# Performance work log

Hardware: AMD Instinct MI355X
Metric: run time of the kernel (lower is better)

The kernel has to match this reference:

```python
import jax, jax.numpy as jnp
import numpy as np

D = 768
H = 16
DH = D // H  # 48
SCALE = 1.0 / np.sqrt(DH).astype(np.float32)
EPS = 1e-3  # keras LayerNormalization default epsilon
NEG = -1e9


def setup_inputs() -> dict:
    key = jax.random.key(0)
    ks = jax.random.split(key, 10)
    B, S = 4, 2048
    q = jax.random.normal(ks[0], (B, S, D), dtype=jnp.float32)
    k = jax.random.normal(ks[1], (B, S, D), dtype=jnp.float32)
    v = jax.random.normal(ks[2], (B, S, D), dtype=jnp.float32)
    # Dense projection params (glorot-ish scale)
    w_std = 1.0 / np.sqrt(D)
    Wq = jax.random.normal(ks[3], (D, D), dtype=jnp.float32) * w_std
    Wk = jax.random.normal(ks[4], (D, D), dtype=jnp.float32) * w_std
    Wv = jax.random.normal(ks[5], (D, D), dtype=jnp.float32) * w_std
    bq = jnp.zeros((D,), jnp.float32)
    bk = jnp.zeros((D,), jnp.float32)
    bv = jnp.zeros((D,), jnp.float32)
    gamma = jnp.ones((D,), jnp.float32)
    beta = jnp.zeros((D,), jnp.float32)
    return {"q": q, "k": k, "v": v, "Wq": Wq, "bq": bq, "Wk": Wk, "bk": bk,
            "Wv": Wv, "bv": bv, "gamma": gamma, "beta": beta}


def reference(q, k, v, Wq, bq, Wk, bk, Wv, bv, gamma, beta):
    use_causal = True  # exercise the causal-mask path
    B, S, _ = q.shape
    # Projections, then split into heads (tf.split on last axis == reshape)
    Q = (q @ Wq + bq).reshape(B, S, H, DH)
    K = (k @ Wk + bk).reshape(B, S, H, DH)
    V = (v @ Wv + bv).reshape(B, S, H, DH)
    # scores: [B, H, Sq, Sk]
    scores = jnp.einsum('bqhd,bkhd->bhqk', Q, K) * SCALE
    if use_causal:
        qi = jnp.arange(S)[:, None]
        ki = jnp.arange(S)[None, :]
        mask = jnp.where(qi >= ki, 0.0, NEG).astype(scores.dtype)
        scores = scores + mask
    attn = jax.nn.softmax(scores, axis=-1)
    out = jnp.einsum('bhqk,bkhd->bqhd', attn, V).reshape(B, S, D)
    # LayerNorm over last dim
    mu = jnp.mean(out, axis=-1, keepdims=True)
    var = jnp.mean(jnp.square(out - mu), axis=-1, keepdims=True)
    return (out - mu) * jax.lax.rsqrt(var + EPS) * gamma + beta
```

## Files before the change

### kernel.cpp

```cpp
#include <hip/hip_runtime.h>
#include <hip/hip_bf16.h>


#define DMODEL 768
#define NHEAD  16
#define DHEAD  48
#define SEQ    2048
#define NBATCH 4
#define NROWS  (NBATCH * SEQ)
#define QSCALE (0.14433756729740643f * 1.4426950408889634f)

typedef __bf16 bf16x8 __attribute__((ext_vector_type(8)));
typedef float  f32x4  __attribute__((ext_vector_type(4)));
typedef float  f32x16 __attribute__((ext_vector_type(16)));
typedef unsigned int u32x4 __attribute__((ext_vector_type(4)));

#if __has_builtin(__builtin_amdgcn_exp2f)
#define EXP2(x) __builtin_amdgcn_exp2f(x)
#else
#define EXP2(x) exp2f(x)
#endif

static __device__ __forceinline__ unsigned int pk2(float lo, float hi) {
    unsigned short a = __builtin_bit_cast(unsigned short, (__bf16)lo);
    unsigned short b = __builtin_bit_cast(unsigned short, (__bf16)hi);
    return ((unsigned int)b << 16) | a;
}

static __device__ __forceinline__ __hip_bfloat16 bfc(float x) {
    return __float2bfloat16(x);
}

__global__ __launch_bounds__(256) void prep(
    const float* __restrict__ Wq,
    const float* __restrict__ Wk,
    const float* __restrict__ Wv,
    const float* __restrict__ xq,
    const float* __restrict__ xk,
    const float* __restrict__ xv,
    __hip_bfloat16* __restrict__ Wt,
    __hip_bfloat16* __restrict__ Xbq,
    __hip_bfloat16* __restrict__ Xbk,
    __hip_bfloat16* __restrict__ Xbv)
{
    int bid = blockIdx.x;
    if (bid < 1728) {
        __shared__ __hip_bfloat16 tile[32][33];
        int mat = bid / 576;
        int t   = bid - mat * 576;
        int tr  = t / 24, tc = t - (t / 24) * 24;
        const float* W = (mat == 0) ? Wq : (mat == 1) ? Wk : Wv;
        __hip_bfloat16* O = Wt + (size_t)mat * DMODEL * DMODEL;
        int tx = threadIdx.x & 31, ty = threadIdx.x >> 5;
#pragma unroll
        for (int i = 0; i < 32; i += 8)
            tile[ty + i][tx] = __float2bfloat16(W[(size_t)(tr * 32 + ty + i) * DMODEL + tc * 32 + tx]);
        __syncthreads();
#pragma unroll
        for (int i = 0; i < 32; i += 8)
            O[(size_t)(tc * 32 + ty + i) * DMODEL + tr * 32 + tx] = tile[tx][ty + i];
    } else {
        int b2  = bid - 1728;
        int mat = b2 / 3072;
        int r   = b2 - mat * 3072;
        const float* X = (mat == 0) ? xq : (mat == 1) ? xk : xv;
        __hip_bfloat16* O = (mat == 0) ? Xbq : (mat == 1) ? Xbk : Xbv;
        size_t off = (size_t)r * 2048 + threadIdx.x * 8;
        float4 f0 = *(const float4*)(X + off);
        float4 f1 = *(const float4*)(X + off + 4);
        unsigned int w0 = pk2(f0.x, f0.y), w1 = pk2(f0.z, f0.w);
        unsigned int w2 = pk2(f1.x, f1.y), w3 = pk2(f1.z, f1.w);
        u32x4 pv; pv[0] = w0; pv[1] = w1; pv[2] = w2; pv[3] = w3;
        *(u32x4*)(O + off) = pv;
    }
}

__global__ __launch_bounds__(512, 4) void qkv_proj(
    const __hip_bfloat16* __restrict__ Xbq,
    const __hip_bfloat16* __restrict__ Xbk,
    const __hip_bfloat16* __restrict__ Xbv,
    const __hip_bfloat16* __restrict__ Wt,
    const float* __restrict__ bq,
    const float* __restrict__ bk,
    const float* __restrict__ bv,
    __hip_bfloat16* __restrict__ Qr,
    __hip_bfloat16* __restrict__ Kr,
    __hip_bfloat16* __restrict__ Vt)
{
    __shared__ __hip_bfloat16 Abuf[3][8192];
    __shared__ __hip_bfloat16 Bbuf[2][4096];

    int tid  = threadIdx.x;
    int w    = tid >> 6, lane = tid & 63;
    int l16  = lane & 15, quad = lane >> 4;
    int wm   = w >> 1, wn = w & 1;

    int xcd = blockIdx.x & 7, s = blockIdx.x >> 3;
    int nt  = s % 6;
    int idx = (s / 6) * 8 + xcd;
    int mat = idx >> 5, mt = idx & 31;
    int m0  = mt * 256, n0 = nt * 128;

    const __hip_bfloat16* X = (mat == 0) ? Xbq : (mat == 1) ? Xbk : Xbv;
    const __hip_bfloat16* W = Wt + (size_t)mat * DMODEL * DMODEL;
    const float* bias       = (mat == 0) ? bq : (mat == 1) ? bk : bv;

    int sr = tid >> 2;
    int sc = ((tid & 3) ^ ((tid >> 3) & 3)) * 8;
    const __hip_bfloat16* ga0 = X + (size_t)(m0 + sr) * DMODEL + sc;
    const __hip_bfloat16* ga1 = X + (size_t)(m0 + 128 + sr) * DMODEL + sc;
    const __hip_bfloat16* gb  = W + (size_t)(n0 + sr) * DMODEL + sc;

#define GLD(gp_, lp_) __builtin_amdgcn_global_load_lds(                        \
        (const __attribute__((address_space(1))) void*)(gp_),                  \
        (__attribute__((address_space(3))) void*)(lp_), 16, 0, 0)

    int swz  = (quad ^ ((l16 >> 1) & 3)) * 8;
    int aoff = (wm * 64 + l16) * 32 + swz;
    int boff = (wn * 64 + l16) * 32 + swz;

    f32x4 acc[4][4] = {};

    GLD(gb,       &Bbuf[0][tid * 8]);
    GLD(ga0,      &Abuf[0][tid * 8]);
    GLD(ga1,      &Abuf[0][4096 + tid * 8]);
    GLD(ga0 + 32, &Abuf[1][tid * 8]);
    GLD(ga1 + 32, &Abuf[1][4096 + tid * 8]);
    asm volatile("s_waitcnt vmcnt(2)" ::: "memory");
    asm volatile("s_barrier" ::: "memory");

    int abuf = 0, bbuf = 0, abS = 2;
    const __hip_bfloat16* gbS  = gb  + 32;
    const __hip_bfloat16* ga0S = ga0 + 64;
    const __hip_bfloat16* ga1S = ga1 + 64;

    for (int kt = 0; kt < 24; ++kt) {
        const __hip_bfloat16* LA = Abuf[abuf];
        const __hip_bfloat16* LB = Bbuf[bbuf];

        bf16x8 a[4], bA[2];
#pragma unroll
        for (int m_ = 0; m_ < 4; ++m_)
            a[m_] = *(const bf16x8*)&LA[aoff + m_ * 512];
        bA[0] = *(const bf16x8*)&LB[boff];
        bA[1] = *(const bf16x8*)&LB[boff + 512];

        if (kt < 23) { GLD(gbS, &Bbuf[bbuf ^ 1][tid * 8]); gbS += 32; }
        if (kt < 22) {
            GLD(ga0S, &Abuf[abS][tid * 8]);
            GLD(ga1S, &Abuf[abS][4096 + tid * 8]);
            ga0S += 32; ga1S += 32;
        }

        asm volatile("s_barrier" ::: "memory");
        __builtin_amdgcn_s_setprio(1);
#pragma unroll
        for (int m_ = 0; m_ < 4; ++m_) {
            acc[m_][0] = __builtin_amdgcn_mfma_f32_16x16x32_bf16(a[m_], bA[0], acc[m_][0], 0, 0, 0);
            acc[m_][1] = __builtin_amdgcn_mfma_f32_16x16x32_bf16(a[m_], bA[1], acc[m_][1], 0, 0, 0);
        }
        __builtin_amdgcn_s_setprio(0);
        asm volatile("s_barrier" ::: "memory");

        bf16x8 bB[2];
        bB[0] = *(const bf16x8*)&LB[boff + 1024];
        bB[1] = *(const bf16x8*)&LB[boff + 1536];

        if (kt < 22) asm volatile("s_waitcnt vmcnt(2)" ::: "memory");
        else         asm volatile("s_waitcnt vmcnt(0)" ::: "memory");
        asm volatile("s_barrier" ::: "memory");
        __builtin_amdgcn_s_setprio(1);
#pragma unroll
        for (int m_ = 0; m_ < 4; ++m_) {
            acc[m_][2] = __builtin_amdgcn_mfma_f32_16x16x32_bf16(a[m_], bB[0], acc[m_][2], 0, 0, 0);
            acc[m_][3] = __builtin_amdgcn_mfma_f32_16x16x32_bf16(a[m_], bB[1], acc[m_][3], 0, 0, 0);
        }
        __builtin_amdgcn_s_setprio(0);
        asm volatile("s_barrier" ::: "memory");

        abuf = (abuf == 2) ? 0 : abuf + 1;
        abS  = (abS  == 2) ? 0 : abS  + 1;
        bbuf ^= 1;
    }
#undef GLD

    int colb = n0 + wn * 64 + l16;
    float bc0 = bias[colb];
    float bc1 = bias[colb + 16];
    float bc2 = bias[colb + 32];
    float bc3 = bias[colb + 48];
    if (mat == 0) {
#pragma unroll
        for (int i = 0; i < 4; ++i) {
            int row0 = m0 + wm * 64 + i * 16 + quad * 4;
#pragma unroll
            for (int r = 0; r < 4; ++r) {
                __hip_bfloat16* p = Qr + (size_t)(row0 + r) * DMODEL + colb;
                p[0]  = bfc((acc[i][0][r] + bc0) * QSCALE);
                p[16] = bfc((acc[i][1][r] + bc1) * QSCALE);
                p[32] = bfc((acc[i][2][r] + bc2) * QSCALE);
                p[48] = bfc((acc[i][3][r] + bc3) * QSCALE);
            }
        }
    } else if (mat == 1) {
#pragma unroll
        for (int i = 0; i < 4; ++i) {
            int row0 = m0 + wm * 64 + i * 16 + quad * 4;
#pragma unroll
            for (int r = 0; r < 4; ++r) {
                __hip_bfloat16* p = Kr + (size_t)(row0 + r) * DMODEL + colb;
                p[0]  = bfc(acc[i][0][r] + bc0);
                p[16] = bfc(acc[i][1][r] + bc1);
                p[32] = bfc(acc[i][2][r] + bc2);
                p[48] = bfc(acc[i][3][r] + bc3);
            }
        }
    } else {
#pragma unroll
        for (int j = 0; j < 4; ++j) {
            int col = colb + j * 16;
            float bc = (j == 0) ? bc0 : (j == 1) ? bc1 : (j == 2) ? bc2 : bc3;
            int h = col / 48, dh = col - h * 48;
#pragma unroll
            for (int i = 0; i < 4; ++i) {
                int row0 = m0 + wm * 64 + i * 16 + quad * 4;
                int bb = row0 >> 11, s0 = row0 & 2047;
                unsigned int lo = pk2(acc[i][j][0] + bc, acc[i][j][1] + bc);
                unsigned int hi = pk2(acc[i][j][2] + bc, acc[i][j][3] + bc);
                uint2 pw; pw.x = lo; pw.y = hi;
                *(uint2*)(Vt + ((size_t)(bb * NHEAD + h) * DHEAD + dh) * SEQ + s0) = pw;
            }
        }
    }
}

__global__ __launch_bounds__(256, 3) void attn(
    const __hip_bfloat16* __restrict__ Qr,
    const __hip_bfloat16* __restrict__ Kr,
    const __hip_bfloat16* __restrict__ Vt,
    __hip_bfloat16* __restrict__ Ao)
{
    __shared__ __hip_bfloat16 Ks[2][64][64];
    __shared__ __hip_bfloat16 Vs[2][64][64];

    int tid  = threadIdx.x;
    int w    = tid >> 6, lane = tid & 63;
    int l31  = lane & 31;
    int half = lane >> 5;
    bool hb  = half != 0;
    int bh   = blockIdx.x & 63;
    int qt   = 15 - (blockIdx.x >> 6);
    int q0   = qt * 128;
    int b    = bh >> 4, h = bh & 15;
    size_t rowbase = (size_t)b * SEQ;

    const __hip_bfloat16* Qp = Qr + rowbase * DMODEL + h * DHEAD;
    const __hip_bfloat16* Kp = Kr + rowbase * DMODEL + h * DHEAD;
    const __hip_bfloat16* Vp = Vt + (size_t)bh * DHEAD * SEQ;

    {
        int zbuf = tid >> 7, zi = tid & 127;
        int zr = 48 + (zi >> 3), zsl = zi & 7;
        unsigned int v = (zr == 48) ? 0x3F803F80u : 0u;
        u32x4 pv; pv[0] = v; pv[1] = v; pv[2] = v; pv[3] = v;
        *(u32x4*)&Vs[zbuf][zr][(zsl ^ (zr & 7)) * 8] = pv;
    }

    int q0w = q0 + w * 32;
    bf16x8 bQ0, bQ1, bQ2;
    {
        const __hip_bfloat16* qp = Qp + (size_t)(q0w + l31) * DMODEL + half * 8;
        bQ0 = *(const bf16x8*)(qp);
        bQ1 = *(const bf16x8*)(qp + 16);
        bQ2 = *(const bf16x8*)(qp + 32);
    }

    int kr1 = tid / 6,          ksl1 = tid - kr1 * 6;
    int kr2 = (tid + 256) / 6,  ksl2 = (tid + 256) - kr2 * 6;
    int vd1 = tid >> 3,         vsl1 = tid & 7;
    int vd2 = (tid + 256) >> 3, vsl2 = tid & 7;
    int kso1 = (ksl1 ^ (kr1 & 7)) * 8;
    int kso2 = (ksl2 ^ (kr2 & 7)) * 8;
    int vso1 = (vsl1 ^ (vd1 & 7)) * 8;
    int vso2 = (vsl2 ^ (vd2 & 7)) * 8;

    const __hip_bfloat16* pK1 = Kp + (size_t)kr1 * DMODEL + ksl1 * 8;
    const __hip_bfloat16* pK2 = Kp + (size_t)kr2 * DMODEL + ksl2 * 8;
    const __hip_bfloat16* pV1 = Vp + (size_t)vd1 * SEQ + vsl1 * 8;
    const __hip_bfloat16* pV2 = Vp + (size_t)vd2 * SEQ + vsl2 * 8;

    uint4 kv1, kv2, vv1, vv2;

#define ATTN_LOAD() {                                                           \
        kv1 = *(const uint4*)pK1;                                               \
        vv1 = *(const uint4*)pV1;                                               \
        if (tid < 128) {                                                        \
            kv2 = *(const uint4*)pK2;                                           \
            vv2 = *(const uint4*)pV2;                                           \
        }                                                                       \
        pK1 += 64 * DMODEL; pK2 += 64 * DMODEL; pV1 += 64; pV2 += 64; }

#define ATTN_STORE(buf_) {                                                      \
        *(uint4*)&Ks[buf_][kr1][kso1] = kv1;                                    \
        *(uint4*)&Vs[buf_][vd1][vso1] = vv1;                                    \
        if (tid < 128) {                                                        \
            *(uint4*)&Ks[buf_][kr2][kso2] = kv2;                                \
            *(uint4*)&Vs[buf_][vd2][vso2] = vv2;                                \
        } }

#define MFMA32(A_, B_, C_) __builtin_amdgcn_mfma_f32_32x32x16_bf16(A_, B_, C_, 0, 0, 0)

    f32x16 O1 = {}, O2 = {};
    const f32x16 z16 = {};

    int ktmax = 2 * qt + 1;
    ATTN_LOAD();
    ATTN_STORE(0);
    ATTN_LOAD();
    __syncthreads();

    for (int kt = 0; kt <= ktmax; ++kt) {
        int buf = kt & 1;
        int k0  = kt * 64;
        if (kt + 1 <= ktmax) ATTN_STORE(buf ^ 1);
        if (kt + 2 <= ktmax) ATTN_LOAD();

#pragma unroll
        for (int kc = 0; kc < 2; ++kc) {
            int kbase = k0 + kc * 32;
            if (kbase <= q0w + 31) {
                int krow = kc * 32 + l31;
                int ksw  = krow & 7;
                bf16x8 aK0 = *(const bf16x8*)&Ks[buf][krow][((0 + half) ^ ksw) * 8];
                bf16x8 aK1 = *(const bf16x8*)&Ks[buf][krow][((2 + half) ^ ksw) * 8];
                bf16x8 aK2 = *(const bf16x8*)&Ks[buf][krow][((4 + half) ^ ksw) * 8];

                __builtin_amdgcn_s_setprio(1);
                f32x16 s_;
                s_ = MFMA32(aK0, bQ0, z16);
                s_ = MFMA32(aK1, bQ1, s_);
                s_ = MFMA32(aK2, bQ2, s_);
                __builtin_amdgcn_s_setprio(0);

                if (kbase + 31 > q0w) {
                    int qg = q0w + l31;
                    int kb = kbase + (hb ? 4 : 0);
#pragma unroll
                    for (int r = 0; r < 16; ++r) {
                        int kl = (r & 3) + 8 * (r >> 2);
                        if (kb + kl > qg) s_[r] = -1e30f;
                    }
                }

                unsigned int p0, p1, p2, p3, p4, p5, p6, p7;
                {
                    float e0 = EXP2(s_[0]),  e1 = EXP2(s_[1]);
                    float e2 = EXP2(s_[2]),  e3 = EXP2(s_[3]);
                    float e4 = EXP2(s_[4]),  e5 = EXP2(s_[5]);
                    float e6 = EXP2(s_[6]),  e7 = EXP2(s_[7]);
                    float e8 = EXP2(s_[8]),  e9 = EXP2(s_[9]);
                    float ea = EXP2(s_[10]), eb = EXP2(s_[11]);
                    float ec = EXP2(s_[12]), ed = EXP2(s_[13]);
                    float ee = EXP2(s_[14]), ef = EXP2(s_[15]);
                    p0 = pk2(e0, e1); p1 = pk2(e2, e3);
                    p2 = pk2(e4, e5); p3 = pk2(e6, e7);
                    p4 = pk2(e8, e9); p5 = pk2(ea, eb);
                    p6 = pk2(ec, ed); p7 = pk2(ee, ef);
                }

                u32x4 F0w, F1w;
#if __has_builtin(__builtin_amdgcn_permlane32_swap)
                {
                    typedef unsigned int u32x2 __attribute__((ext_vector_type(2)));
                    u32x2 r0 = __builtin_amdgcn_permlane32_swap(p0, p2, false, false);
                    u32x2 r1 = __builtin_amdgcn_permlane32_swap(p1, p3, false, false);
                    u32x2 r2 = __builtin_amdgcn_permlane32_swap(p4, p6, false, false);
                    u32x2 r3 = __builtin_amdgcn_permlane32_swap(p5, p7, false, false);
                    F0w[0] = r0[0]; F0w[1] = r1[0]; F0w[2] = r0[1]; F0w[3] = r1[1];
                    F1w[0] = r2[0]; F1w[1] = r3[0]; F1w[2] = r2[1]; F1w[3] = r3[1];
                }
#else
                {
                    unsigned int sx0 = __shfl_xor(hb ? p0 : p2, 32, 64);
                    unsigned int sx1 = __shfl_xor(hb ? p1 : p3, 32, 64);
                    unsigned int sx2 = __shfl_xor(hb ? p4 : p6, 32, 64);
                    unsigned int sx3 = __shfl_xor(hb ? p5 : p7, 32, 64);
                    F0w[0] = hb ? sx0 : p0;  F0w[1] = hb ? sx1 : p1;
                    F0w[2] = hb ? p2  : sx0; F0w[3] = hb ? p3  : sx1;
                    F1w[0] = hb ? sx2 : p4;  F1w[1] = hb ? sx3 : p5;
                    F1w[2] = hb ? p6  : sx2; F1w[3] = hb ? p7  : sx3;
                }
#endif
                bf16x8 F0 = __builtin_bit_cast(bf16x8, F0w);
                bf16x8 F1 = __builtin_bit_cast(bf16x8, F1w);

                int vr0 = l31, vr1 = 32 + l31;
                int vw0 = vr0 & 7, vw1 = vr1 & 7;
                bf16x8 bV00 = *(const bf16x8*)&Vs[buf][vr0][((kc * 4 + 0 + half) ^ vw0) * 8];
                bf16x8 bV01 = *(const bf16x8*)&Vs[buf][vr1][((kc * 4 + 0 + half) ^ vw1) * 8];
                bf16x8 bV10 = *(const bf16x8*)&Vs[buf][vr0][((kc * 4 + 2 + half) ^ vw0) * 8];
                bf16x8 bV11 = *(const bf16x8*)&Vs[buf][vr1][((kc * 4 + 2 + half) ^ vw1) * 8];

                __builtin_amdgcn_s_setprio(1);
                O1 = MFMA32(F0, bV00, O1);
                O2 = MFMA32(F0, bV01, O2);
                O1 = MFMA32(F1, bV10, O1);
                O2 = MFMA32(F1, bV11, O2);
                __builtin_amdgcn_s_setprio(0);
            }
        }

        asm volatile("s_waitcnt lgkmcnt(0)" ::: "memory");
        __builtin_amdgcn_s_barrier();
        asm volatile("" ::: "memory");
    }

    int lsrc = (lane & 32) + 16;
#pragma unroll
    for (int r = 0; r < 16; ++r) {
        float lden = __shfl(O2[r], lsrc, 64);
        float linv = 1.f / lden;
        int q = q0w + (r & 3) + 8 * (r >> 2) + (hb ? 4 : 0);
        size_t g = (rowbase + q) * DMODEL + h * DHEAD;
        Ao[g + l31] = __float2bfloat16(O1[r] * linv);
        if (l31 < 16)
            Ao[g + 32 + l31] = __float2bfloat16(O2[r] * linv);
    }
#undef ATTN_LOAD
#undef ATTN_STORE
#undef MFMA32
}

__global__ __launch_bounds__(256) void lnorm(
    const __hip_bfloat16* __restrict__ Ao,
    const float* __restrict__ gamma,
    const float* __restrict__ beta,
    float* __restrict__ out)
{
    int tid = threadIdx.x;
    int wv  = tid >> 6, ln = tid & 63;
    int row = blockIdx.x * 4 + wv;
    size_t base = (size_t)row * DMODEL + ln * 4;

    ushort4 u0 = *(const ushort4*)(Ao + base);
    ushort4 u1 = *(const ushort4*)(Ao + base + 256);
    ushort4 u2 = *(const ushort4*)(Ao + base + 512);
    float x0, x1, x2, x3, x4, x5, x6, x7, x8, x9, xa, xb;
    { unsigned int v = (unsigned int)u0.x << 16; __builtin_memcpy(&x0, &v, 4); }
    { unsigned int v = (unsigned int)u0.y << 16; __builtin_memcpy(&x1, &v, 4); }
    { unsigned int v = (unsigned int)u0.z << 16; __builtin_memcpy(&x2, &v, 4); }
    { unsigned int v = (unsigned int)u0.w << 16; __builtin_memcpy(&x3, &v, 4); }
    { unsigned int v = (unsigned int)u1.x << 16; __builtin_memcpy(&x4, &v, 4); }
    { unsigned int v = (unsigned int)u1.y << 16; __builtin_memcpy(&x5, &v, 4); }
    { unsigned int v = (unsigned int)u1.z << 16; __builtin_memcpy(&x6, &v, 4); }
    { unsigned int v = (unsigned int)u1.w << 16; __builtin_memcpy(&x7, &v, 4); }
    { unsigned int v = (unsigned int)u2.x << 16; __builtin_memcpy(&x8, &v, 4); }
    { unsigned int v = (unsigned int)u2.y << 16; __builtin_memcpy(&x9, &v, 4); }
    { unsigned int v = (unsigned int)u2.z << 16; __builtin_memcpy(&xa, &v, 4); }
    { unsigned int v = (unsigned int)u2.w << 16; __builtin_memcpy(&xb, &v, 4); }

    float s = ((x0 + x1) + (x2 + x3)) + ((x4 + x5) + (x6 + x7)) + ((x8 + x9) + (xa + xb));
    float q = ((x0*x0 + x1*x1) + (x2*x2 + x3*x3)) + ((x4*x4 + x5*x5) + (x6*x6 + x7*x7))
            + ((x8*x8 + x9*x9) + (xa*xa + xb*xb));
#pragma unroll
    for (int m = 32; m >= 1; m >>= 1) {
        s += __shfl_xor(s, m, 64);
        q += __shfl_xor(q, m, 64);
    }
    float mu  = s * (1.f / 768.f);
    float var = q * (1.f / 768.f) - mu * mu;
    float rstd = rsqrtf(var + 1e-3f);

    float4 g0 = *(const float4*)(gamma + ln * 4);
    float4 g1 = *(const float4*)(gamma + ln * 4 + 256);
    float4 g2 = *(const float4*)(gamma + ln * 4 + 512);
    float4 e0 = *(const float4*)(beta + ln * 4);
    float4 e1 = *(const float4*)(beta + ln * 4 + 256);
    float4 e2 = *(const float4*)(beta + ln * 4 + 512);
    float4 o0, o1, o2;
    o0.x = (x0 - mu) * rstd * g0.x + e0.x;
    o0.y = (x1 - mu) * rstd * g0.y + e0.y;
    o0.z = (x2 - mu) * rstd * g0.z + e0.z;
    o0.w = (x3 - mu) * rstd * g0.w + e0.w;
    o1.x = (x4 - mu) * rstd * g1.x + e1.x;
    o1.y = (x5 - mu) * rstd * g1.y + e1.y;
    o1.z = (x6 - mu) * rstd * g1.z + e1.z;
    o1.w = (x7 - mu) * rstd * g1.w + e1.w;
    o2.x = (x8 - mu) * rstd * g2.x + e2.x;
    o2.y = (x9 - mu) * rstd * g2.y + e2.y;
    o2.z = (xa - mu) * rstd * g2.z + e2.z;
    o2.w = (xb - mu) * rstd * g2.w + e2.w;
    *(float4*)(out + base)       = o0;
    *(float4*)(out + base + 256) = o1;
    *(float4*)(out + base + 512) = o2;
}

extern "C" void kernel_launch(void* const* d_in, const int* in_sizes, int n_in,
                              void* d_out, int out_size, void* d_ws, size_t ws_size,
                              hipStream_t stream) {
    const float* q     = (const float*)d_in[0];
    const float* k     = (const float*)d_in[1];
    const float* v     = (const float*)d_in[2];
    const float* Wq    = (const float*)d_in[3];
    const float* bq    = (const float*)d_in[4];
    const float* Wk    = (const float*)d_in[5];
    const float* bk    = (const float*)d_in[6];
    const float* Wv    = (const float*)d_in[7];
    const float* bv    = (const float*)d_in[8];
    const float* gamma = (const float*)d_in[9];
    const float* beta  = (const float*)d_in[10];

    char* basep = (char*)d_ws;
    __hip_bfloat16* Wt = (__hip_bfloat16*)basep;
    __hip_bfloat16* Qr = (__hip_bfloat16*)(basep + 3538944);
    __hip_bfloat16* Kr = Qr + (size_t)NROWS * DMODEL;
    __hip_bfloat16* Vt = Kr + (size_t)NROWS * DMODEL;
    __hip_bfloat16* Ao = Vt + (size_t)NROWS * DMODEL;
    float* out = (float*)d_out;

    __hip_bfloat16* Xbq = (__hip_bfloat16*)d_out;
    __hip_bfloat16* Xbk = Xbq + (size_t)NROWS * DMODEL;
    __hip_bfloat16* Xbv = Ao;

    hipLaunchKernelGGL(prep, dim3(10944), dim3(256), 0, stream,
                       Wq, Wk, Wv, q, k, v, Wt, Xbq, Xbk, Xbv);
    hipLaunchKernelGGL(qkv_proj, dim3(576), dim3(512), 0, stream,
                       Xbq, Xbk, Xbv, Wt, bq, bk, bv, Qr, Kr, Vt);
    hipLaunchKernelGGL(attn, dim3(1024), dim3(256), 0, stream, Qr, Kr, Vt, Ao);
    hipLaunchKernelGGL(lnorm, dim3(2048), dim3(256), 0, stream, Ao, gamma, beta, out);
}
```

Before: 233.4 us.

## Shrink QKV projection tiles to 128x128 with 256-thread blocks and simplify pipeline

The QKV projection GEMM moves from 256x128 tiles on 512-thread blocks to 128x128 tiles on 256-thread blocks, doubling the grid to 1152 blocks. Each wave now loads all four B fragments at once and issues 16 MFMAs per k-step, and the four barriers per iteration become one. The aim is better occupancy, fewer wasted barrier stalls and better load balance across CUs. The cost is less reuse of the weight tile per block, so more global and L2 traffic for B.

```diff
diff --git a/kernel.cpp b/kernel.cpp
--- a/kernel.cpp
+++ b/kernel.cpp
@@ -75,7 +75,7 @@
     }
 }
 
-__global__ __launch_bounds__(512, 4) void qkv_proj(
+__global__ __launch_bounds__(256, 4) void qkv_proj(
     const __hip_bfloat16* __restrict__ Xbq,
     const __hip_bfloat16* __restrict__ Xbk,
     const __hip_bfloat16* __restrict__ Xbv,
@@ -87,7 +87,7 @@
     __hip_bfloat16* __restrict__ Kr,
     __hip_bfloat16* __restrict__ Vt)
 {
-    __shared__ __hip_bfloat16 Abuf[3][8192];
+    __shared__ __hip_bfloat16 Abuf[3][4096];
     __shared__ __hip_bfloat16 Bbuf[2][4096];
 
     int tid  = threadIdx.x;
@@ -98,8 +98,8 @@
     int xcd = blockIdx.x & 7, s = blockIdx.x >> 3;
     int nt  = s % 6;
     int idx = (s / 6) * 8 + xcd;
-    int mat = idx >> 5, mt = idx & 31;
-    int m0  = mt * 256, n0 = nt * 128;
+    int mat = idx >> 6, mt = idx & 63;
+    int m0  = mt * 128, n0 = nt * 128;
 
     const __hip_bfloat16* X = (mat == 0) ? Xbq : (mat == 1) ? Xbk : Xbv;
     const __hip_bfloat16* W = Wt + (size_t)mat * DMODEL * DMODEL;
@@ -107,13 +107,18 @@
 
     int sr = tid >> 2;
     int sc = ((tid & 3) ^ ((tid >> 3) & 3)) * 8;
-    const __hip_bfloat16* ga0 = X + (size_t)(m0 + sr) * DMODEL + sc;
-    const __hip_bfloat16* ga1 = X + (size_t)(m0 + 128 + sr) * DMODEL + sc;
-    const __hip_bfloat16* gb  = W + (size_t)(n0 + sr) * DMODEL + sc;
+    const __hip_bfloat16* ga = X + (size_t)(m0 + sr) * DMODEL + sc;
+    const __hip_bfloat16* gb = W + (size_t)(n0 + sr) * DMODEL + sc;
 
 #define GLD(gp_, lp_) __builtin_amdgcn_global_load_lds(                        \
         (const __attribute__((address_space(1))) void*)(gp_),                  \
         (__attribute__((address_space(3))) void*)(lp_), 16, 0, 0)
+#define GLDB(t_, buf_) {                                                       \
+        GLD(gb + (t_) * 32,               &Bbuf[buf_][tid * 8]);               \
+        GLD(gb + 64 * DMODEL + (t_) * 32, &Bbuf[buf_][2048 + tid * 8]); }
+#define GLDA(t_, buf_) {                                                       \
+        GLD(ga + (t_) * 32,               &Abuf[buf_][tid * 8]);               \
+        GLD(ga + 64 * DMODEL + (t_) * 32, &Abuf[buf_][2048 + tid * 8]); }
 
     int swz  = (quad ^ ((l16 >> 1) & 3)) * 8;
     int aoff = (wm * 64 + l16) * 32 + swz;
@@ -121,68 +126,50 @@
 
     f32x4 acc[4][4] = {};
 
-    GLD(gb,       &Bbuf[0][tid * 8]);
-    GLD(ga0,      &Abuf[0][tid * 8]);
-    GLD(ga1,      &Abuf[0][4096 + tid * 8]);
-    GLD(ga0 + 32, &Abuf[1][tid * 8]);
-    GLD(ga1 + 32, &Abuf[1][4096 + tid * 8]);
+    GLDB(0, 0);
+    GLDA(0, 0);
+    GLDA(1, 1);
     asm volatile("s_waitcnt vmcnt(2)" ::: "memory");
     asm volatile("s_barrier" ::: "memory");
 
-    int abuf = 0, bbuf = 0, abS = 2;
-    const __hip_bfloat16* gbS  = gb  + 32;
-    const __hip_bfloat16* ga0S = ga0 + 64;
-    const __hip_bfloat16* ga1S = ga1 + 64;
-
+    int ab = 0, bb = 0;
     for (int kt = 0; kt < 24; ++kt) {
-        const __hip_bfloat16* LA = Abuf[abuf];
-        const __hip_bfloat16* LB = Bbuf[bbuf];
-
-        bf16x8 a[4], bA[2];
-#pragma unroll
-        for (int m_ = 0; m_ < 4; ++m_)
-            a[m_] = *(const bf16x8*)&LA[aoff + m_ * 512];
-        bA[0] = *(const bf16x8*)&LB[boff];
-        bA[1] = *(const bf16x8*)&LB[boff + 512];
-
-        if (kt < 23) { GLD(gbS, &Bbuf[bbuf ^ 1][tid * 8]); gbS += 32; }
-        if (kt < 22) {
-            GLD(ga0S, &Abuf[abS][tid * 8]);
-            GLD(ga1S, &Abuf[abS][4096 + tid * 8]);
-            ga0S += 32; ga1S += 32;
+        const __hip_bfloat16* LA = Abuf[ab];
+        const __hip_bfloat16* LB = Bbuf[bb];
+
+        bf16x8 a[4], b[4];
+#pragma unroll
+        for (int i = 0; i < 4; ++i)
+            a[i] = *(const bf16x8*)&LA[aoff + i * 512];
+#pragma unroll
+        for (int j = 0; j < 4; ++j)
+            b[j] = *(const bf16x8*)&LB[boff + j * 512];
+
+        if (kt < 23) GLDB(kt + 1, bb ^ 1);
+        int aw = (ab == 0) ? 2 : ab - 1;
+        if (kt < 22) GLDA(kt + 2, aw);
+
+        __builtin_amdgcn_s_setprio(1);
+#pragma unroll
+        for (int i = 0; i < 4; ++i)
+#pragma unroll
+            for (int j = 0; j < 4; ++j)
+                acc[i][j] = __builtin_amdgcn_mfma_f32_16x16x32_bf16(a[i], b[j], acc[i][j], 0, 0, 0);
+        __builtin_amdgcn_s_setprio(0);
+
+        if (kt < 23) {
+            asm volatile("s_waitcnt lgkmcnt(0)" ::: "memory");
+            if (kt < 22) asm volatile("s_waitcnt vmcnt(2)" ::: "memory");
+            else         asm volatile("s_waitcnt vmcnt(0)" ::: "memory");
+            asm volatile("s_barrier" ::: "memory");
         }
 
-        asm volatile("s_barrier" ::: "memory");
-        __builtin_amdgcn_s_setprio(1);
-#pragma unroll
-        for (int m_ = 0; m_ < 4; ++m_) {
-            acc[m_][0] = __builtin_amdgcn_mfma_f32_16x16x32_bf16(a[m_], bA[0], acc[m_][0], 0, 0, 0);
-            acc[m_][1] = __builtin_amdgcn_mfma_f32_16x16x32_bf16(a[m_], bA[1], acc[m_][1], 0, 0, 0);
-        }
-        __builtin_amdgcn_s_setprio(0);
-        asm volatile("s_barrier" ::: "memory");
-
-        bf16x8 bB[2];
-        bB[0] = *(const bf16x8*)&LB[boff + 1024];
-        bB[1] = *(const bf16x8*)&LB[boff + 1536];
-
-        if (kt < 22) asm volatile("s_waitcnt vmcnt(2)" ::: "memory");
-        else         asm volatile("s_waitcnt vmcnt(0)" ::: "memory");
-        asm volatile("s_barrier" ::: "memory");
-        __builtin_amdgcn_s_setprio(1);
-#pragma unroll
-        for (int m_ = 0; m_ < 4; ++m_) {
-            acc[m_][2] = __builtin_amdgcn_mfma_f32_16x16x32_bf16(a[m_], bB[0], acc[m_][2], 0, 0, 0);
-            acc[m_][3] = __builtin_amdgcn_mfma_f32_16x16x32_bf16(a[m_], bB[1], acc[m_][3], 0, 0, 0);
-        }
-        __builtin_amdgcn_s_setprio(0);
-        asm volatile("s_barrier" ::: "memory");
-
-        abuf = (abuf == 2) ? 0 : abuf + 1;
-        abS  = (abS  == 2) ? 0 : abS  + 1;
-        bbuf ^= 1;
+        ab = (ab == 2) ? 0 : ab + 1;
+        bb ^= 1;
     }
 #undef GLD
+#undef GLDA
+#undef GLDB
 
     int colb = n0 + wn * 64 + l16;
     float bc0 = bias[colb];
@@ -224,11 +211,11 @@
 #pragma unroll
             for (int i = 0; i < 4; ++i) {
                 int row0 = m0 + wm * 64 + i * 16 + quad * 4;
-                int bb = row0 >> 11, s0 = row0 & 2047;
+                int bb2 = row0 >> 11, s0 = row0 & 2047;
                 unsigned int lo = pk2(acc[i][j][0] + bc, acc[i][j][1] + bc);
                 unsigned int hi = pk2(acc[i][j][2] + bc, acc[i][j][3] + bc);
                 uint2 pw; pw.x = lo; pw.y = hi;
-                *(uint2*)(Vt + ((size_t)(bb * NHEAD + h) * DHEAD + dh) * SEQ + s0) = pw;
+                *(uint2*)(Vt + ((size_t)(bb2 * NHEAD + h) * DHEAD + dh) * SEQ + s0) = pw;
             }
         }
     }
@@ -524,7 +511,7 @@
 
     hipLaunchKernelGGL(prep, dim3(10944), dim3(256), 0, stream,
                        Wq, Wk, Wv, q, k, v, Wt, Xbq, Xbk, Xbv);
-    hipLaunchKernelGGL(qkv_proj, dim3(576), dim3(512), 0, stream,
+    hipLaunchKernelGGL(qkv_proj, dim3(1152), dim3(256), 0, stream,
                        Xbq, Xbk, Xbv, Wt, bq, bk, bv, Qr, Kr, Vt);
     hipLaunchKernelGGL(attn, dim3(1024), dim3(256), 0, stream, Qr, Kr, Vt, Ao);
     hipLaunchKernelGGL(lnorm, dim3(2048), dim3(256), 0, stream, Ao, gamma, beta, out);
```

After: 225.4 us. 3.4% less time.
